# Kernel optimization log

Hardware: AMD Instinct MI355X
Metric: run time of the kernel (lower is better)

Reference implementation:

```python
import jax, jax.numpy as jnp
import numpy as np

NUM_USER = 50000
NUM_ITEM = 50000
DIM_FEAT = 4096
DIM_LATENT = 128
NUM_LAYER = 2
AVG_DEG = 16
N = NUM_USER + NUM_ITEM
E_HALF = NUM_USER * AVG_DEG  # user->item edges; reversed copies added too


def setup_inputs() -> dict:
    key = jax.random.key(0)
    ks = jax.random.split(key, 6)
    features = jax.random.normal(ks[0], (NUM_ITEM, DIM_FEAT), dtype=jnp.float32)
    # xavier_normal for preference: std = sqrt(2/(fan_in+fan_out))
    preference = jax.random.normal(ks[1], (NUM_USER, DIM_LATENT), dtype=jnp.float32) * np.sqrt(2.0 / (NUM_USER + DIM_LATENT)).astype(np.float32)
    W1 = jax.random.normal(ks[2], (DIM_FEAT, 4 * DIM_LATENT), dtype=jnp.float32) * np.float32(DIM_FEAT ** -0.5)
    b1 = jnp.zeros((4 * DIM_LATENT,), jnp.float32)
    W2 = jax.random.normal(ks[3], (4 * DIM_LATENT, DIM_LATENT), dtype=jnp.float32) * np.float32((4 * DIM_LATENT) ** -0.5)
    b2 = jnp.zeros((DIM_LATENT,), jnp.float32)
    # bipartite user-item edges, both directions; no self-loops by construction
    u = jax.random.randint(ks[4], (E_HALF,), 0, NUM_USER)
    it = jax.random.randint(ks[5], (E_HALF,), NUM_USER, N)
    src = jnp.concatenate([u, it])
    dst = jnp.concatenate([it, u])
    edge_index = jnp.stack([src, dst], axis=0)
    return {"features": features, "preference": preference, "W1": W1, "b1": b1,
            "W2": W2, "b2": b2, "edge_index": edge_index}


def reference(features, preference, W1, b1, W2, b2, edge_index):
    # proj MLP: Linear -> LeakyReLU(0.01) -> Linear
    item_feat = jax.nn.leaky_relu(features @ W1 + b1, negative_slope=0.01) @ W2 + b2
    x = jnp.concatenate([preference, item_feat], axis=0)  # [N, D]
    # F.normalize(x, dim=-1): divide by L2 norm clamped to 1e-12
    x = x / jnp.maximum(jnp.linalg.norm(x, axis=-1, keepdims=True), 1e-12)
    row, col = edge_index[0], edge_index[1]  # source (j), target (i)
    # degree over source index only, as in BaseGCN.message
    deg = jax.ops.segment_sum(jnp.ones(row.shape[0], dtype=x.dtype), row, num_segments=N)
    deg_inv_sqrt = deg ** -0.5  # endpoints all appear as sources, so finite on edges
    norm = deg_inv_sqrt[row] * deg_inv_sqrt[col]  # [E]
    out = x
    h = x
    for _ in range(NUM_LAYER):
        msg = norm[:, None] * h[row]                      # gather + scale [E, D]
        h = jax.ops.segment_sum(msg, col, num_segments=N)  # scatter-add [N, D]
        out = out + h
    return out, preference
```

## Files before the change

kernel.cpp:

```cpp
#include <hip/hip_runtime.h>

#define NUSER 50000
#define NITEM 50000
#define NTOT  100000
#define DFEAT 4096
#define DLAT  128
#define DHID  512
#define MTILES 391
#define MPAD  (MTILES*128)
#define G1TILES 782

typedef __attribute__((ext_vector_type(8))) short bf16x8;
typedef __attribute__((ext_vector_type(4))) float f32x4;

__device__ __forceinline__ ushort f2bf(float f) {
  union { float f; unsigned u; } in; in.f = f;
  unsigned u = in.u;
  u += 0x7fffu + ((u >> 16) & 1u);
  return (ushort)(u >> 16);
}
__device__ __forceinline__ unsigned pk2bf_fast(float lo, float hi) {
  unsigned ul = __float_as_uint(lo) + 0x8000u;
  unsigned uh = __float_as_uint(hi) + 0x8000u;
  return (ul >> 16) | (uh & 0xffff0000u);
}
__device__ __forceinline__ float bflo(unsigned u) { return __uint_as_float(u << 16); }
__device__ __forceinline__ float bfhi(unsigned u) { return __uint_as_float(u & 0xffff0000u); }

__global__ __launch_bounds__(512, 4) void gemm1_kernel(
    const float* __restrict__ A,
    const ushort* __restrict__ BT,
    const float* __restrict__ bias,
    ushort* __restrict__ Hid)
{
  extern __shared__ char smem[];
  char* AsC = smem;
  char* BsC = smem + 8192;

  const int tid = threadIdx.x;
  const int lane = tid & 63;
  const int wid = tid >> 6;
  const int row0 = blockIdx.x * 64;

  const int lr = lane & 15;
  const int kq = lane >> 4;
  const int l7 = lane & 7;

  f32x4 acc[4][4];
  const f32x4 z = {0.f, 0.f, 0.f, 0.f};
  #pragma unroll
  for (int m = 0; m < 4; ++m)
    #pragma unroll
    for (int n = 0; n < 4; ++n) acc[m][n] = z;

  const int r0 = tid >> 3, t0 = tid & 7;
  const int aoff = r0 * 128 + ((t0 ^ (r0 & 7)) << 4);
  const size_t asrc = (size_t)(row0 + r0) * DFEAT + t0 * 8;
  const bool aok = (row0 + r0) < NITEM;

  for (int k0 = 0; k0 < DFEAT; k0 += 64) {
    #pragma unroll
    for (int j = 0; j < 8; ++j) {
      int q = (wid * 8 + j) * 64 + lane;
      int r = q >> 3, t = q & 7;
      const ushort* src = BT + (size_t)r * DFEAT + k0 + ((t ^ (r & 7)) << 3);
      __builtin_amdgcn_global_load_lds(
          (const __attribute__((address_space(1))) void*)src,
          (__attribute__((address_space(3))) void*)(BsC + (size_t)(wid * 8 + j) * 1024),
          16, 0, 0);
    }
    {
      float4 v0 = make_float4(0.f, 0.f, 0.f, 0.f), v1 = v0;
      if (aok) {
        const float* s = A + asrc + k0;
        v0 = *(const float4*)s; v1 = *(const float4*)(s + 4);
      }
      uint4 p;
      p.x = pk2bf_fast(v0.x, v0.y); p.y = pk2bf_fast(v0.z, v0.w);
      p.z = pk2bf_fast(v1.x, v1.y); p.w = pk2bf_fast(v1.z, v1.w);
      *(uint4*)(AsC + aoff) = p;
    }
    __syncthreads();

    #pragma unroll
    for (int kk = 0; kk < 2; ++kk) {
      const int c8 = kk * 4 + kq;
      const int sx = (c8 ^ l7) << 4;
      bf16x8 a[4], b[4];
      #pragma unroll
      for (int m = 0; m < 4; ++m)
        a[m] = *(const bf16x8*)(AsC + (m * 16 + lr) * 128 + sx);
      #pragma unroll
      for (int n = 0; n < 4; ++n)
        b[n] = *(const bf16x8*)(BsC + (wid * 64 + n * 16 + lr) * 128 + sx);
      #pragma unroll
      for (int m = 0; m < 4; ++m)
        #pragma unroll
        for (int n = 0; n < 4; ++n)
          acc[m][n] = __builtin_amdgcn_mfma_f32_16x16x32_bf16(a[m], b[n], acc[m][n], 0, 0, 0);
    }
    __syncthreads();
  }

  #pragma unroll
  for (int n = 0; n < 4; ++n) {
    int col = wid * 64 + n * 16 + lr;
    float bv = bias[col];
    #pragma unroll
    for (int m = 0; m < 4; ++m) {
      #pragma unroll
      for (int i = 0; i < 4; ++i) {
        int row = row0 + m * 16 + kq * 4 + i;
        float v = acc[m][n][i] + bv;
        v = v > 0.f ? v : 0.01f * v;
        Hid[(size_t)row * DHID + col] = f2bf(v);
      }
    }
  }
}

#define BM 128
#define BK 32
#define LDW 40

__global__ __launch_bounds__(256, 4) void gemm2_kernel(
    const ushort* __restrict__ A,
    const ushort* __restrict__ BT,
    const float* __restrict__ bias,
    float* __restrict__ X)
{
  __shared__ ushort As[BM][LDW];
  __shared__ ushort Bs[BM][LDW];
  const int tid = threadIdx.x;
  const int lane = tid & 63;
  const int wid = tid >> 6;
  const int wr = wid >> 1, wc = wid & 1;
  const int row0 = blockIdx.x * BM;

  f32x4 acc[4][4];
  const f32x4 z = {0.f, 0.f, 0.f, 0.f};
  #pragma unroll
  for (int m = 0; m < 4; ++m)
    #pragma unroll
    for (int n = 0; n < 4; ++n) acc[m][n] = z;

  const int lrow = lane & 15;
  const int kb = (lane >> 4) * 8;

  for (int k0 = 0; k0 < DHID; k0 += BK) {
    #pragma unroll
    for (int j = 0; j < 2; ++j) {
      int idx = tid + j * 256;
      int r = idx >> 2;
      int c8 = (idx & 3) << 3;
      *(uint4*)&As[r][c8] = *(const uint4*)(A + (size_t)(row0 + r) * DHID + k0 + c8);
      *(uint4*)&Bs[r][c8] = *(const uint4*)(BT + (size_t)r * DHID + k0 + c8);
    }
    __syncthreads();
    bf16x8 a[4], b[4];
    #pragma unroll
    for (int m = 0; m < 4; ++m) a[m] = *(const bf16x8*)&As[wr * 64 + m * 16 + lrow][kb];
    #pragma unroll
    for (int n = 0; n < 4; ++n) b[n] = *(const bf16x8*)&Bs[wc * 64 + n * 16 + lrow][kb];
    #pragma unroll
    for (int m = 0; m < 4; ++m)
      #pragma unroll
      for (int n = 0; n < 4; ++n)
        acc[m][n] = __builtin_amdgcn_mfma_f32_16x16x32_bf16(a[m], b[n], acc[m][n], 0, 0, 0);
    __syncthreads();
  }
  #pragma unroll
  for (int n = 0; n < 4; ++n) {
    int col = wc * 64 + n * 16 + lrow;
    float bv = bias[col];
    #pragma unroll
    for (int m = 0; m < 4; ++m) {
      #pragma unroll
      for (int i = 0; i < 4; ++i) {
        int row = row0 + wr * 64 + m * 16 + (lane >> 4) * 4 + i;
        if (row < NITEM)
          X[(size_t)(NUSER + row) * DLAT + col] = acc[m][n][i] + bv;
      }
    }
  }
}

__global__ __launch_bounds__(256) void prep_w1t(const float* __restrict__ W1,
                                                ushort* __restrict__ W1T) {
  __shared__ ushort t[64][72];
  const int bx = blockIdx.x & 63;
  const int by = blockIdx.x >> 6;
  const int k0 = bx * 64, n0 = by * 64;
  const int tid = threadIdx.x;
  #pragma unroll
  for (int j = 0; j < 4; ++j) {
    int f = tid + j * 256;
    int r = f >> 4, c4 = (f & 15) << 2;
    float4 v = *(const float4*)(W1 + (size_t)(k0 + r) * DHID + n0 + c4);
    t[c4 + 0][r] = f2bf(v.x);
    t[c4 + 1][r] = f2bf(v.y);
    t[c4 + 2][r] = f2bf(v.z);
    t[c4 + 3][r] = f2bf(v.w);
  }
  __syncthreads();
  #pragma unroll
  for (int j = 0; j < 2; ++j) {
    int o = tid + j * 256;
    int r = o >> 3, c8 = (o & 7) << 3;
    *(uint4*)(W1T + (size_t)(n0 + r) * DFEAT + k0 + c8) = *(const uint4*)&t[r][c8];
  }
}
__global__ void prep_w2t(const float* __restrict__ W2, ushort* __restrict__ W2T) {
  int idx = blockIdx.x * 256 + threadIdx.x;
  int n = idx >> 9, k = idx & 511;
  W2T[idx] = f2bf(W2[(size_t)k * DLAT + n]);
}

__global__ __launch_bounds__(256) void normalize_kernel(
    const float* __restrict__ pref, float* __restrict__ X,
    unsigned* __restrict__ Xb) {
  int gw = (blockIdx.x * 256 + threadIdx.x) >> 6;
  int lane = threadIdx.x & 63;
  if (gw >= NTOT) return;
  const float* src = (gw < NUSER) ? (pref + (size_t)gw * DLAT) : (X + (size_t)gw * DLAT);
  float2 v = *(const float2*)(src + lane * 2);
  float s = v.x * v.x + v.y * v.y;
  #pragma unroll
  for (int off = 32; off; off >>= 1) s += __shfl_xor(s, off, 64);
  float inv = 1.0f / fmaxf(sqrtf(s), 1e-12f);
  float2 o; o.x = v.x * inv; o.y = v.y * inv;
  *(float2*)(X + (size_t)gw * DLAT + lane * 2) = o;
  Xb[(size_t)gw * 64 + lane] = pk2bf_fast(o.x, o.y);
}

__global__ void count_kernel(const int* __restrict__ col, int* __restrict__ cnt, int E) {
  int e = blockIdx.x * 256 + threadIdx.x;
  if (e < E) atomicAdd(&cnt[col[e]], 1);
}
__global__ void dinv_kernel(const int* __restrict__ cnt, float* __restrict__ dinv, int n) {
  int i = blockIdx.x * 256 + threadIdx.x;
  if (i < n) dinv[i] = rsqrtf((float)cnt[i]);
}

#define SCAN_NB ((NTOT + 1023) / 1024)
__global__ __launch_bounds__(1024) void scan1_kernel(const int* __restrict__ cnt,
                                                     int* __restrict__ off,
                                                     int* __restrict__ bsum, int n) {
  __shared__ int ws[16];
  __shared__ int wexcl[16];
  const int tid = threadIdx.x, lane = tid & 63, wv = tid >> 6;
  int i = blockIdx.x * 1024 + tid;
  int v = (i < n) ? cnt[i] : 0;
  int x = v;
  #pragma unroll
  for (int o = 1; o < 64; o <<= 1) {
    int t = __shfl_up(x, o, 64);
    if (lane >= o) x += t;
  }
  if (lane == 63) ws[wv] = x;
  __syncthreads();
  if (tid < 16) {
    int y = ws[tid];
    #pragma unroll
    for (int o = 1; o < 16; o <<= 1) {
      int t = __shfl_up(y, o, 64);
      if (tid >= o) y += t;
    }
    wexcl[tid] = y - ws[tid];
    if (tid == 15) bsum[blockIdx.x] = y;
  }
  __syncthreads();
  if (i < n) off[i] = wexcl[wv] + (x - v);
}
__global__ __launch_bounds__(128) void scan2_kernel(int* __restrict__ bsum,
                                                    int* __restrict__ off, int nb, int n) {
  __shared__ int ws[2];
  const int tid = threadIdx.x, lane = tid & 63, wv = tid >> 6;
  int v = (tid < nb) ? bsum[tid] : 0;
  int x = v;
  #pragma unroll
  for (int o = 1; o < 64; o <<= 1) {
    int t = __shfl_up(x, o, 64);
    if (lane >= o) x += t;
  }
  if (lane == 63) ws[wv] = x;
  __syncthreads();
  int excl_w = (wv == 1) ? ws[0] : 0;
  if (tid < nb) bsum[tid] = excl_w + (x - v);
  if (tid == nb - 1) off[n] = excl_w + x;
}
__global__ __launch_bounds__(1024) void scan3_kernel(int* __restrict__ off,
                                                     const int* __restrict__ bsum, int n) {
  int i = blockIdx.x * 1024 + threadIdx.x;
  if (i < n) off[i] += bsum[blockIdx.x];
}

__global__ void fill_kernel(const int* __restrict__ row, const int* __restrict__ col,
                            const float* __restrict__ dinv, const int* __restrict__ off,
                            int* __restrict__ cur, int2* __restrict__ srcw, int E) {
  int e = blockIdx.x * 256 + threadIdx.x;
  if (e >= E) return;
  int r = row[e], c = col[e];
  float w = dinv[r] * dinv[c];
  int p = atomicAdd(&cur[c], 1);
  int2 pk; pk.x = r; pk.y = __float_as_int(w);
  srcw[off[c] + p] = pk;
}

template <int FINAL>
__global__ __launch_bounds__(256) void spmm_kernel(
    const int2* __restrict__ srcw, const int* __restrict__ off,
    const unsigned* __restrict__ hb, float* __restrict__ hout,
    unsigned* __restrict__ houtb,
    const float* __restrict__ addA, const float* __restrict__ addB) {
  int node = (int)((blockIdx.x * 256 + threadIdx.x) >> 6);
  int lane = threadIdx.x & 63;
  if (node >= NTOT) return;
  int p = off[node], pend = off[node + 1];
  float ax = 0.f, ay = 0.f;
  for (; p + 3 < pend; p += 4) {
    int2 e0 = srcw[p];
    int2 e1 = srcw[p + 1];
    int2 e2 = srcw[p + 2];
    int2 e3 = srcw[p + 3];
    unsigned u0 = hb[(size_t)e0.x * 64 + lane];
    unsigned u1 = hb[(size_t)e1.x * 64 + lane];
    unsigned u2 = hb[(size_t)e2.x * 64 + lane];
    unsigned u3 = hb[(size_t)e3.x * 64 + lane];
    float w0 = __int_as_float(e0.y), w1 = __int_as_float(e1.y);
    float w2 = __int_as_float(e2.y), w3 = __int_as_float(e3.y);
    ax += w0 * bflo(u0) + w1 * bflo(u1) + w2 * bflo(u2) + w3 * bflo(u3);
    ay += w0 * bfhi(u0) + w1 * bfhi(u1) + w2 * bfhi(u2) + w3 * bfhi(u3);
  }
  for (; p < pend; ++p) {
    int2 e0 = srcw[p];
    float w0 = __int_as_float(e0.y);
    unsigned u0 = hb[(size_t)e0.x * 64 + lane];
    ax += w0 * bflo(u0);
    ay += w0 * bfhi(u0);
  }
  size_t o = (size_t)node * DLAT + lane * 2;
  if (FINAL) {
    float2 a = *(const float2*)(addA + o);
    float2 b = *(const float2*)(addB + o);
    ax += a.x + b.x;
    ay += a.y + b.y;
  } else {
    houtb[(size_t)node * 64 + lane] = pk2bf_fast(ax, ay);
  }
  float2 r; r.x = ax; r.y = ay;
  *(float2*)(hout + o) = r;
}

extern "C" void kernel_launch(void* const* d_in, const int* in_sizes, int n_in,
                              void* d_out, int out_size, void* d_ws, size_t ws_size,
                              hipStream_t stream) {
  const float* features  = (const float*)d_in[0];
  const float* preference = (const float*)d_in[1];
  const float* W1 = (const float*)d_in[2];
  const float* b1 = (const float*)d_in[3];
  const float* W2 = (const float*)d_in[4];
  const float* b2 = (const float*)d_in[5];
  const int*   edges = (const int*)d_in[6];
  const int E = in_sizes[6] / 2;
  const int* erow = edges;
  const int* ecol = edges + E;
  float* out = (float*)d_out;

  char* ws = (char*)d_ws;
  size_t off_b = 0;
  auto alloc = [&](size_t bytes) {
    void* p = ws + off_b;
    off_b = (off_b + bytes + 255) & ~(size_t)255;
    return p;
  };
  ushort*   W1T  = (ushort*)alloc((size_t)DHID * DFEAT * 2);
  ushort*   W2T  = (ushort*)alloc((size_t)DLAT * DHID * 2);
  ushort*   Hid  = (ushort*)alloc((size_t)MPAD * DHID * 2);
  float*    X    = (float*)alloc((size_t)NTOT * DLAT * 4);
  float*    hA   = (float*)alloc((size_t)NTOT * DLAT * 4);
  unsigned* Xb   = (unsigned*)alloc((size_t)NTOT * 64 * 4);
  unsigned* hAb  = (unsigned*)alloc((size_t)NTOT * 64 * 4);
  int*      cnt  = (int*)alloc((size_t)NTOT * 4);
  int*      offs = (int*)alloc((size_t)(NTOT + 1) * 4);
  int*      cur  = (int*)alloc((size_t)NTOT * 4);
  float*    dinv = (float*)alloc((size_t)NTOT * 4);
  int*      bsum = (int*)alloc((size_t)SCAN_NB * 4);
  int2*     srcw = (int2*)alloc((size_t)E * 8);

  prep_w1t<<<512, 256, 0, stream>>>(W1, W1T);
  prep_w2t<<<(DLAT * DHID) / 256, 256, 0, stream>>>(W2, W2T);
  gemm1_kernel<<<G1TILES, 512, 72 * 1024, stream>>>(features, W1T, b1, Hid);
  gemm2_kernel<<<MTILES, 256, 0, stream>>>(Hid, W2T, b2, X);
  normalize_kernel<<<(NTOT * 64 + 255) / 256, 256, 0, stream>>>(preference, X, Xb);

  hipMemsetAsync(cnt, 0, (size_t)NTOT * 4, stream);
  count_kernel<<<(E + 255) / 256, 256, 0, stream>>>(ecol, cnt, E);
  dinv_kernel<<<(NTOT + 255) / 256, 256, 0, stream>>>(cnt, dinv, NTOT);
  scan1_kernel<<<SCAN_NB, 1024, 0, stream>>>(cnt, offs, bsum, NTOT);
  scan2_kernel<<<1, 128, 0, stream>>>(bsum, offs, SCAN_NB, NTOT);
  scan3_kernel<<<SCAN_NB, 1024, 0, stream>>>(offs, bsum, NTOT);
  hipMemsetAsync(cur, 0, (size_t)NTOT * 4, stream);
  fill_kernel<<<(E + 255) / 256, 256, 0, stream>>>(erow, ecol, dinv, offs, cur, srcw, E);

  spmm_kernel<0><<<(NTOT * 64 + 255) / 256, 256, 0, stream>>>(srcw, offs, Xb, hA, hAb, nullptr, nullptr);
  spmm_kernel<1><<<(NTOT * 64 + 255) / 256, 256, 0, stream>>>(srcw, offs, hAb, out, nullptr, X, hA);

  hipMemcpyAsync(out + (size_t)NTOT * DLAT, preference, (size_t)NUSER * DLAT * 4,
                 hipMemcpyDeviceToDevice, stream);
}
```

Measured before the change: 750.6 us.

## Double-buffer LDS tiles in gemm1 to overlap global loads with MFMA

Restructures the gemm1 main loop into a two-stage software pipeline. The next k-tile's B data is loaded asynchronously into a second LDS buffer, and its A data is prefetched into registers, while the current tile is computed. Manual barriers and waitcnt replace the two __syncthreads per iteration, and the out-of-range row guard becomes a clamped row index. LDS use doubles to 144KB, which limits occupancy to one block per CU; launch_bounds is lowered to match.

```diff
diff --git a/kernel.cpp b/kernel.cpp
--- a/kernel.cpp
+++ b/kernel.cpp
@@ -27,15 +27,17 @@
 __device__ __forceinline__ float bflo(unsigned u) { return __uint_as_float(u << 16); }
 __device__ __forceinline__ float bfhi(unsigned u) { return __uint_as_float(u & 0xffff0000u); }
 
-__global__ __launch_bounds__(512, 4) void gemm1_kernel(
+__global__ __launch_bounds__(512, 2) void gemm1_kernel(
     const float* __restrict__ A,
     const ushort* __restrict__ BT,
     const float* __restrict__ bias,
     ushort* __restrict__ Hid)
 {
   extern __shared__ char smem[];
-  char* AsC = smem;
-  char* BsC = smem + 8192;
+  char* const As0 = smem;
+  char* const As1 = smem + 8192;
+  char* const Bs0 = smem + 16384;
+  char* const Bs1 = smem + 16384 + 65536;
 
   const int tid = threadIdx.x;
   const int lane = tid & 63;
@@ -55,10 +57,10 @@
 
   const int r0 = tid >> 3, t0 = tid & 7;
   const int aoff = r0 * 128 + ((t0 ^ (r0 & 7)) << 4);
-  const size_t asrc = (size_t)(row0 + r0) * DFEAT + t0 * 8;
-  const bool aok = (row0 + r0) < NITEM;
-
-  for (int k0 = 0; k0 < DFEAT; k0 += 64) {
+  const int arow = min(row0 + r0, NITEM - 1);
+  const float* aptr = A + (size_t)arow * DFEAT + t0 * 8;
+
+  auto issueB = [&](char* dstB, int k0) {
     #pragma unroll
     for (int j = 0; j < 8; ++j) {
       int q = (wid * 8 + j) * 64 + lane;
@@ -66,22 +68,11 @@
       const ushort* src = BT + (size_t)r * DFEAT + k0 + ((t ^ (r & 7)) << 3);
       __builtin_amdgcn_global_load_lds(
           (const __attribute__((address_space(1))) void*)src,
-          (__attribute__((address_space(3))) void*)(BsC + (size_t)(wid * 8 + j) * 1024),
+          (__attribute__((address_space(3))) void*)(dstB + (size_t)(wid * 8 + j) * 1024),
           16, 0, 0);
     }
-    {
-      float4 v0 = make_float4(0.f, 0.f, 0.f, 0.f), v1 = v0;
-      if (aok) {
-        const float* s = A + asrc + k0;
-        v0 = *(const float4*)s; v1 = *(const float4*)(s + 4);
-      }
-      uint4 p;
-      p.x = pk2bf_fast(v0.x, v0.y); p.y = pk2bf_fast(v0.z, v0.w);
-      p.z = pk2bf_fast(v1.x, v1.y); p.w = pk2bf_fast(v1.z, v1.w);
-      *(uint4*)(AsC + aoff) = p;
-    }
-    __syncthreads();
-
+  };
+  auto compute = [&](const char* AsC, const char* BsC) {
     #pragma unroll
     for (int kk = 0; kk < 2; ++kk) {
       const int c8 = kk * 4 + kq;
@@ -99,7 +90,43 @@
         for (int n = 0; n < 4; ++n)
           acc[m][n] = __builtin_amdgcn_mfma_f32_16x16x32_bf16(a[m], b[n], acc[m][n], 0, 0, 0);
     }
-    __syncthreads();
+  };
+
+  float4 c0, c1;
+
+  auto iterstep = [&](int t, char* Asc, char* Bsc, char* Asn, char* Bsn) {
+    __builtin_amdgcn_s_barrier();
+    __builtin_amdgcn_sched_barrier(0);
+    float4 n0 = {0.f, 0.f, 0.f, 0.f}, n1 = n0;
+    if (t < 63) {
+      const float* s = aptr + (size_t)(t + 1) * 64;
+      n0 = *(const float4*)s;
+      n1 = *(const float4*)(s + 4);
+      issueB(Bsn, (t + 1) * 64);
+      asm volatile("s_waitcnt vmcnt(10)" ::: "memory");
+    } else {
+      asm volatile("s_waitcnt vmcnt(0)" ::: "memory");
+    }
+    __builtin_amdgcn_sched_barrier(0);
+    uint4 p;
+    p.x = pk2bf_fast(c0.x, c0.y); p.y = pk2bf_fast(c0.z, c0.w);
+    p.z = pk2bf_fast(c1.x, c1.y); p.w = pk2bf_fast(c1.z, c1.w);
+    *(uint4*)(Asc + aoff) = p;
+    asm volatile("s_waitcnt lgkmcnt(0)" ::: "memory");
+    __builtin_amdgcn_s_barrier();
+    __builtin_amdgcn_sched_barrier(0);
+    compute(Asc, Bsc);
+    __builtin_amdgcn_sched_barrier(0);
+    c0 = n0; c1 = n1;
+  };
+
+  c0 = *(const float4*)aptr;
+  c1 = *(const float4*)(aptr + 4);
+  issueB(Bs0, 0);
+
+  for (int t = 0; t < 64; t += 2) {
+    iterstep(t,     As0, Bs0, As1, Bs1);
+    iterstep(t + 1, As1, Bs1, As0, Bs0);
   }
 
   #pragma unroll
@@ -390,7 +417,7 @@
 
   prep_w1t<<<512, 256, 0, stream>>>(W1, W1T);
   prep_w2t<<<(DLAT * DHID) / 256, 256, 0, stream>>>(W2, W2T);
-  gemm1_kernel<<<G1TILES, 512, 72 * 1024, stream>>>(features, W1T, b1, Hid);
+  gemm1_kernel<<<G1TILES, 512, 144 * 1024, stream>>>(features, W1T, b1, Hid);
   gemm2_kernel<<<MTILES, 256, 0, stream>>>(Hid, W2T, b2, X);
   normalize_kernel<<<(NTOT * 64 + 255) / 256, 256, 0, stream>>>(preference, X, Xb);
 
```

Result: slower. 935.8 us (+24.7%).

## Fuse item L2 normalization into gemm2 epilogue and drop fp32 layer-1 buffer

Applied to the files above, without the earlier changes.

The gemm2 epilogue now computes per-row squared norms with shuffles and shared memory, normalizes the item rows, and writes both fp32 X and packed bf16 Xb. The separate normalize pass therefore only handles user rows. The first SpMM layer no longer writes an fp32 hidden buffer, and the final layer adds the bf16 copy of layer 1 instead. This removes a full read and write of the item half of X plus one fp32 NxD write and read, at the cost of extra epilogue syncs and slightly lower precision for the layer-1 term.

```diff
diff --git a/kernel.cpp b/kernel.cpp
--- a/kernel.cpp
+++ b/kernel.cpp
@@ -127,10 +127,12 @@
     const ushort* __restrict__ A,
     const ushort* __restrict__ BT,
     const float* __restrict__ bias,
-    float* __restrict__ X)
+    float* __restrict__ X,
+    unsigned* __restrict__ Xb)
 {
   __shared__ ushort As[BM][LDW];
   __shared__ ushort Bs[BM][LDW];
+  __shared__ float rsum[BM];
   const int tid = threadIdx.x;
   const int lane = tid & 63;
   const int wid = tid >> 6;
@@ -145,7 +147,8 @@
     for (int n = 0; n < 4; ++n) acc[m][n] = z;
 
   const int lrow = lane & 15;
-  const int kb = (lane >> 4) * 8;
+  const int kq = lane >> 4;
+  const int kb = kq * 8;
 
   for (int k0 = 0; k0 < DHID; k0 += BK) {
     #pragma unroll
@@ -169,6 +172,47 @@
         acc[m][n] = __builtin_amdgcn_mfma_f32_16x16x32_bf16(a[m], b[n], acc[m][n], 0, 0, 0);
     __syncthreads();
   }
+
+  float prt[4][4];
+  #pragma unroll
+  for (int m = 0; m < 4; ++m)
+    #pragma unroll
+    for (int i = 0; i < 4; ++i) prt[m][i] = 0.f;
+  #pragma unroll
+  for (int n = 0; n < 4; ++n) {
+    float bv = bias[wc * 64 + n * 16 + lrow];
+    #pragma unroll
+    for (int m = 0; m < 4; ++m)
+      #pragma unroll
+      for (int i = 0; i < 4; ++i) {
+        float v = acc[m][n][i] + bv;
+        prt[m][i] += v * v;
+      }
+  }
+  #pragma unroll
+  for (int msk = 1; msk < 16; msk <<= 1)
+    #pragma unroll
+    for (int m = 0; m < 4; ++m)
+      #pragma unroll
+      for (int i = 0; i < 4; ++i)
+        prt[m][i] += __shfl_xor(prt[m][i], msk, 64);
+  if (wc == 0 && lrow == 0) {
+    #pragma unroll
+    for (int m = 0; m < 4; ++m)
+      #pragma unroll
+      for (int i = 0; i < 4; ++i)
+        rsum[wr * 64 + m * 16 + kq * 4 + i] = prt[m][i];
+  }
+  __syncthreads();
+  if (wc == 1 && lrow == 0) {
+    #pragma unroll
+    for (int m = 0; m < 4; ++m)
+      #pragma unroll
+      for (int i = 0; i < 4; ++i)
+        rsum[wr * 64 + m * 16 + kq * 4 + i] += prt[m][i];
+  }
+  __syncthreads();
+
   #pragma unroll
   for (int n = 0; n < 4; ++n) {
     int col = wc * 64 + n * 16 + lrow;
@@ -177,9 +221,17 @@
     for (int m = 0; m < 4; ++m) {
       #pragma unroll
       for (int i = 0; i < 4; ++i) {
-        int row = row0 + wr * 64 + m * 16 + (lane >> 4) * 4 + i;
-        if (row < NITEM)
-          X[(size_t)(NUSER + row) * DLAT + col] = acc[m][n][i] + bv;
+        int rl = wr * 64 + m * 16 + kq * 4 + i;
+        int row = row0 + rl;
+        float inv = rsqrtf(fmaxf(rsum[rl], 1e-24f));
+        float v = (acc[m][n][i] + bv) * inv;
+        float vo = __shfl_xor(v, 1, 64);
+        if (row < NITEM) {
+          size_t node = (size_t)(NUSER + row);
+          X[node * DLAT + col] = v;
+          if ((lrow & 1) == 0)
+            Xb[node * 64 + (col >> 1)] = pk2bf_fast(v, vo);
+        }
       }
     }
   }
@@ -216,14 +268,13 @@
   W2T[idx] = f2bf(W2[(size_t)k * DLAT + n]);
 }
 
-__global__ __launch_bounds__(256) void normalize_kernel(
+__global__ __launch_bounds__(256) void normalize_pref(
     const float* __restrict__ pref, float* __restrict__ X,
     unsigned* __restrict__ Xb) {
   int gw = (blockIdx.x * 256 + threadIdx.x) >> 6;
   int lane = threadIdx.x & 63;
-  if (gw >= NTOT) return;
-  const float* src = (gw < NUSER) ? (pref + (size_t)gw * DLAT) : (X + (size_t)gw * DLAT);
-  float2 v = *(const float2*)(src + lane * 2);
+  if (gw >= NUSER) return;
+  float2 v = *(const float2*)(pref + (size_t)gw * DLAT + lane * 2);
   float s = v.x * v.x + v.y * v.y;
   #pragma unroll
   for (int off = 32; off; off >>= 1) s += __shfl_xor(s, off, 64);
@@ -312,7 +363,7 @@
     const int2* __restrict__ srcw, const int* __restrict__ off,
     const unsigned* __restrict__ hb, float* __restrict__ hout,
     unsigned* __restrict__ houtb,
-    const float* __restrict__ addA, const float* __restrict__ addB) {
+    const float* __restrict__ addX, const unsigned* __restrict__ addH1) {
   int node = (int)((blockIdx.x * 256 + threadIdx.x) >> 6);
   int lane = threadIdx.x & 63;
   if (node >= NTOT) return;
@@ -339,17 +390,17 @@
     ax += w0 * bflo(u0);
     ay += w0 * bfhi(u0);
   }
-  size_t o = (size_t)node * DLAT + lane * 2;
   if (FINAL) {
-    float2 a = *(const float2*)(addA + o);
-    float2 b = *(const float2*)(addB + o);
-    ax += a.x + b.x;
-    ay += a.y + b.y;
+    size_t o = (size_t)node * DLAT + lane * 2;
+    float2 a = *(const float2*)(addX + o);
+    unsigned h1 = addH1[(size_t)node * 64 + lane];
+    ax += a.x + bflo(h1);
+    ay += a.y + bfhi(h1);
+    float2 r; r.x = ax; r.y = ay;
+    *(float2*)(hout + o) = r;
   } else {
     houtb[(size_t)node * 64 + lane] = pk2bf_fast(ax, ay);
   }
-  float2 r; r.x = ax; r.y = ay;
-  *(float2*)(hout + o) = r;
 }
 
 extern "C" void kernel_launch(void* const* d_in, const int* in_sizes, int n_in,
@@ -378,7 +429,6 @@
   ushort*   W2T  = (ushort*)alloc((size_t)DLAT * DHID * 2);
   ushort*   Hid  = (ushort*)alloc((size_t)MPAD * DHID * 2);
   float*    X    = (float*)alloc((size_t)NTOT * DLAT * 4);
-  float*    hA   = (float*)alloc((size_t)NTOT * DLAT * 4);
   unsigned* Xb   = (unsigned*)alloc((size_t)NTOT * 64 * 4);
   unsigned* hAb  = (unsigned*)alloc((size_t)NTOT * 64 * 4);
   int*      cnt  = (int*)alloc((size_t)NTOT * 4);
@@ -391,8 +441,8 @@
   prep_w1t<<<512, 256, 0, stream>>>(W1, W1T);
   prep_w2t<<<(DLAT * DHID) / 256, 256, 0, stream>>>(W2, W2T);
   gemm1_kernel<<<G1TILES, 512, 72 * 1024, stream>>>(features, W1T, b1, Hid);
-  gemm2_kernel<<<MTILES, 256, 0, stream>>>(Hid, W2T, b2, X);
-  normalize_kernel<<<(NTOT * 64 + 255) / 256, 256, 0, stream>>>(preference, X, Xb);
+  gemm2_kernel<<<MTILES, 256, 0, stream>>>(Hid, W2T, b2, X, Xb);
+  normalize_pref<<<(NUSER * 64 + 255) / 256, 256, 0, stream>>>(preference, X, Xb);
 
   hipMemsetAsync(cnt, 0, (size_t)NTOT * 4, stream);
   count_kernel<<<(E + 255) / 256, 256, 0, stream>>>(ecol, cnt, E);
@@ -403,8 +453,8 @@
   hipMemsetAsync(cur, 0, (size_t)NTOT * 4, stream);
   fill_kernel<<<(E + 255) / 256, 256, 0, stream>>>(erow, ecol, dinv, offs, cur, srcw, E);
 
-  spmm_kernel<0><<<(NTOT * 64 + 255) / 256, 256, 0, stream>>>(srcw, offs, Xb, hA, hAb, nullptr, nullptr);
-  spmm_kernel<1><<<(NTOT * 64 + 255) / 256, 256, 0, stream>>>(srcw, offs, hAb, out, nullptr, X, hA);
+  spmm_kernel<0><<<(NTOT * 64 + 255) / 256, 256, 0, stream>>>(srcw, offs, Xb, nullptr, hAb, nullptr, nullptr);
+  spmm_kernel<1><<<(NTOT * 64 + 255) / 256, 256, 0, stream>>>(srcw, offs, hAb, out, nullptr, X, hAb);
 
   hipMemcpyAsync(out + (size_t)NTOT * DLAT, preference, (size_t)NUSER * DLAT * 4,
                  hipMemcpyDeviceToDevice, stream);
```

New measurement: 738.9 us. No clear change (-1.6%).
